# Kernel optimization log

Measured on AMD Instinct MI355X. Metric: run time of the kernel, lower is better.

The kernel has to match this reference:

```python
import jax, jax.numpy as jnp
import numpy as np

N_NODES = 50000
N_EDGES = 400000
F_IN = 128
HID = 64
HEADS = 8
N_CLASSES = 16
NEG_SLOPE = 0.2  # PyG GATConv default negative_slope


def _glorot(key, shape):
    fan_in, fan_out = shape[0], shape[-1]
    lim = jnp.sqrt(6.0 / (fan_in + fan_out))
    return jax.random.uniform(key, shape, jnp.float32, -lim, lim)


def setup_inputs() -> dict:
    key = jax.random.key(0)
    ks = jax.random.split(key, 16)
    x = jax.random.normal(ks[0], (N_NODES, F_IN), jnp.float32)
    edge_index = jax.random.randint(ks[1], (2, N_EDGES), 0, N_NODES, jnp.int64)
    # layer 0: F_IN -> HEADS*HID (concat)
    W0 = _glorot(ks[2], (F_IN, HEADS * HID))
    a_s0 = _glorot(ks[3], (HEADS, HID))
    a_d0 = _glorot(ks[4], (HEADS, HID))
    b0 = jnp.zeros((HEADS * HID,), jnp.float32)
    # layer 1: HEADS*HID -> HEADS*HID (concat)
    W1 = _glorot(ks[5], (HEADS * HID, HEADS * HID))
    a_s1 = _glorot(ks[6], (HEADS, HID))
    a_d1 = _glorot(ks[7], (HEADS, HID))
    b1 = jnp.zeros((HEADS * HID,), jnp.float32)
    # final layer: HEADS*HID -> N_CLASSES, heads=1, concat=False (mean over heads)
    W2 = _glorot(ks[8], (HEADS * HID, 1 * N_CLASSES))
    a_s2 = _glorot(ks[9], (1, N_CLASSES))
    a_d2 = _glorot(ks[10], (1, N_CLASSES))
    b2 = jnp.zeros((N_CLASSES,), jnp.float32)
    return {"x": x, "edge_index": edge_index,
            "W0": W0, "a_s0": a_s0, "a_d0": a_d0, "b0": b0,
            "W1": W1, "a_s1": a_s1, "a_d1": a_d1, "b1": b1,
            "W2": W2, "a_s2": a_s2, "a_d2": a_d2, "b2": b2}


def gat_conv(x, src, dst, W, a_src, a_dst, b, num_nodes, concat):
    """One PyG-style GATConv (self-loops already in src/dst).
    x: [N, F_in]; W: [F_in, H*C]; a_src/a_dst: [H, C]; b: [H*C] or [C]."""
    H, C = a_src.shape
    h = (x @ W).reshape(num_nodes, H, C)                    # [N,H,C]
    al_s = jnp.einsum('nhc,hc->nh', h, a_src)               # [N,H]
    al_d = jnp.einsum('nhc,hc->nh', h, a_dst)               # [N,H]
    e = jax.nn.leaky_relu(al_s[src] + al_d[dst], NEG_SLOPE) # [E,H]
    # scatter-softmax over incoming edges of each destination node
    m = jax.ops.segment_max(e, dst, num_segments=num_nodes)  # [N,H]
    ex = jnp.exp(e - m[dst])
    denom = jax.ops.segment_sum(ex, dst, num_segments=num_nodes)
    alpha = ex / denom[dst]                                  # [E,H]
    out = jax.ops.segment_sum(alpha[:, :, None] * h[src], dst,
                              num_segments=num_nodes)        # [N,H,C]
    if concat:
        return out.reshape(num_nodes, H * C) + b
    return out.mean(axis=1) + b


def reference(x, edge_index, W0, a_s0, a_d0, b0, W1, a_s1, a_d1, b1,
              W2, a_s2, a_d2, b2):
    N = x.shape[0]
    # PyG GATConv adds self-loops by default
    loops = jnp.arange(N, dtype=edge_index.dtype)
    src = jnp.concatenate([edge_index[0], loops])
    dst = jnp.concatenate([edge_index[1], loops])
    h = gat_conv(x, src, dst, W0, a_s0, a_d0, b0, N, concat=True)
    h = jax.nn.elu(h)  # dropout is identity in eval mode
    h = gat_conv(h, src, dst, W1, a_s1, a_d1, b1, N, concat=True)
    h = jax.nn.elu(h)
    return gat_conv(h, src, dst, W2, a_s2, a_d2, b2, N, concat=False)
```

## Files before the change

kernel.cpp:

```cpp
#include <hip/hip_runtime.h>

#define N_NODES 50000
#define N_EDGES 400000
#define E_TOT   450000
#define NEG 0.2f
#define NB_SCAN ((N_NODES + 255) / 256)
#define MAXD 64

typedef unsigned short ushort_t;
typedef __attribute__((ext_vector_type(8))) _Float16 half8;
typedef __attribute__((ext_vector_type(4))) float  f32x4;
typedef __attribute__((ext_vector_type(8))) unsigned short ushort8;

__device__ __forceinline__ ushort_t f2h(float f){
    _Float16 h = (_Float16)f;
    union { _Float16 h; ushort_t u; } v; v.h = h; return v.u;
}
__device__ __forceinline__ float h_lo(unsigned u){
    union { unsigned u; _Float16 h[2]; } v; v.u = u; return (float)v.h[0];
}
__device__ __forceinline__ float h_hi(unsigned u){
    union { unsigned u; _Float16 h[2]; } v; v.u = u; return (float)v.h[1];
}
__device__ __forceinline__ void gload_lds16(const void* g, void* l){
    __builtin_amdgcn_global_load_lds((const __attribute__((address_space(1))) void*)g,
                                     (__attribute__((address_space(3))) void*)l, 16, 0, 0);
}
__device__ __forceinline__ int wave_incl_scan(int v, int lane){
    #pragma unroll
    for(int off = 1; off < 64; off <<= 1){
        int t = __shfl_up(v, off, 64);
        if(lane >= off) v += t;
    }
    return v;
}


__global__ void cvt_all(const float* __restrict__ x, const float* __restrict__ W0,
                        const float* __restrict__ W1, const float* __restrict__ W2,
                        const int* __restrict__ ei,
                        ushort_t* __restrict__ xbf, ushort_t* __restrict__ W0t,
                        ushort_t* __restrict__ W1t, ushort_t* __restrict__ W2t,
                        int* __restrict__ deg){
    int i = blockIdx.x*256 + threadIdx.x;
    if(i < N_NODES*128) xbf[i] = f2h(x[i]);
    if(i < 512*128){ int n = i >> 7, k = i & 127; W0t[i] = f2h(W0[(size_t)k*512 + n]); }
    if(i < 512*512){ int n = i >> 9, k = i & 511; W1t[i] = f2h(W1[(size_t)k*512 + n]); }
    if(i < 16*512){ int n = i >> 9, k = i & 511; W2t[i] = f2h(W2[(size_t)k*16 + n]); }
    if(i < E_TOT){
        int dst = (i < N_EDGES) ? ei[N_EDGES + i] : (i - N_EDGES);
        atomicAdd(&deg[dst], 1);
    }
}


__global__ void alloc_rows(int* __restrict__ wofs, int* __restrict__ rs, int* __restrict__ re){
    int i = blockIdx.x*256 + threadIdx.x;
    int lane = threadIdx.x & 63;
    int d = (i < N_NODES) ? wofs[i] : 0;
    int incl = wave_incl_scan(d, lane);
    int tot = __shfl(incl, 63);
    int base;
    if(lane == 63) base = atomicAdd(&wofs[N_NODES], tot);
    base = __shfl(base, 63);
    int start = base + incl - d;
    if(i < N_NODES){ rs[i] = start; re[i] = start + d; wofs[i] = start; }
}

__global__ void scatter_edges(const int* __restrict__ ei, int* __restrict__ wofs,
                              int* __restrict__ csr){
    int e = blockIdx.x*256 + threadIdx.x;
    if(e >= E_TOT) return;
    int src, dst;
    if(e < N_EDGES){ src = ei[e]; dst = ei[N_EDGES + e]; }
    else { src = dst = e - N_EDGES; }
    int pos = atomicAdd(&wofs[dst], 1);
    csr[pos] = src;
}


template<int K>
__global__ __launch_bounds__(512, 2) void gemm_bt8(const ushort_t* __restrict__ A,
                                                   const ushort_t* __restrict__ Bt,
                                                   ushort_t* __restrict__ Cb,
                                                   const float* __restrict__ a_s,
                                                   const float* __restrict__ a_d,
                                                   float* __restrict__ als,
                                                   float* __restrict__ ald, int M){
    extern __shared__ ushort_t lds[];
    constexpr int NT = K / 64;
    int tid = threadIdx.x, wave = tid >> 6, lane = tid & 63;
    int wm = wave >> 2, wn = wave & 3;
    int row0 = blockIdx.y * 256;
    int col0 = blockIdx.x * 256;

    int lr = lane >> 3;
    int cs8 = ((lane & 7) ^ lr) << 3;
    int arows[4], brows[4];
    #pragma unroll
    for(int i = 0; i < 4; i++){
        int r = row0 + (wave << 5) + (i << 3) + lr;
        arows[i] = r < M ? r : M-1;
        brows[i] = col0 + (wave << 5) + (i << 3) + lr;
    }

    int l15 = lane & 15, fq = lane >> 4;
    int xr = (lane & 7) << 4;
    int xco0 = ((fq << 4)      ) ^ xr;
    int xco1 = (64 | (fq << 4)) ^ xr;

    f32x4 acc[8][4] = {};

    auto stage = [&](int nb, int kt, int i){
        ushort_t* la = lds + nb*16384 + (wave << 11) + (i << 9);
        ushort_t* lb = lds + 32768 + nb*16384 + (wave << 11) + (i << 9);
        gload_lds16(A  + (size_t)arows[i]*K + kt + cs8, la);
        gload_lds16(Bt + (size_t)brows[i]*K + kt + cs8, lb);
    };

    #pragma unroll
    for(int i = 0; i < 4; i++) stage(0, 0, i);

    for(int it = 0; it < NT; ++it){
        int b = it & 1;
        asm volatile("s_waitcnt vmcnt(0)" ::: "memory");
        __builtin_amdgcn_s_barrier();
        const char* Ac = (const char*)(lds + b*16384);
        const char* Bc = (const char*)(lds + 32768 + b*16384);
        #pragma unroll
        for(int p = 0; p < 4; ++p){
            if(it < NT-1 && p < 2){
                stage(b ^ 1, (it + 1) << 6, 2*p);
                stage(b ^ 1, (it + 1) << 6, 2*p + 1);
            }
            half8 aF[2][2], bF[4][2];
            #pragma unroll
            for(int m2 = 0; m2 < 2; m2++){
                int ro = (((wm << 7) + (((p << 1) | m2) << 4) + l15)) << 7;
                aF[m2][0] = *(const half8*)(Ac + ro + xco0);
                aF[m2][1] = *(const half8*)(Ac + ro + xco1);
            }
            #pragma unroll
            for(int nj = 0; nj < 4; nj++){
                int ro = (((wn << 6) + (nj << 4) + l15)) << 7;
                bF[nj][0] = *(const half8*)(Bc + ro + xco0);
                bF[nj][1] = *(const half8*)(Bc + ro + xco1);
            }
            __builtin_amdgcn_s_barrier();
            __builtin_amdgcn_s_setprio(1);
            #pragma unroll
            for(int m2 = 0; m2 < 2; m2++)
                #pragma unroll
                for(int nj = 0; nj < 4; nj++){
                    acc[(p<<1)|m2][nj] = __builtin_amdgcn_mfma_f32_16x16x32_f16(aF[m2][0], bF[nj][0], acc[(p<<1)|m2][nj], 0, 0, 0);
                    acc[(p<<1)|m2][nj] = __builtin_amdgcn_mfma_f32_16x16x32_f16(aF[m2][1], bF[nj][1], acc[(p<<1)|m2][nj], 0, 0, 0);
                }
            __builtin_amdgcn_s_setprio(0);
            __builtin_amdgcn_s_barrier();
        }
    }

    int head = (col0 >> 6) + wn;
    float asv[4], adv[4];
    #pragma unroll
    for(int nj = 0; nj < 4; nj++){
        int c = (head << 6) + (nj << 4) + l15;
        asv[nj] = a_s[c]; adv[nj] = a_d[c];
    }
    #pragma unroll
    for(int mi = 0; mi < 8; mi++){
        #pragma unroll
        for(int p2 = 0; p2 < 4; p2++){
            int r = row0 + (wm << 7) + (mi << 4) + (fq << 2) + p2;
            float ps = 0.f, pd = 0.f;
            if(r < M){
                ushort_t* cp = &Cb[(size_t)r*512 + (head << 6) + l15];
                #pragma unroll
                for(int nj = 0; nj < 4; nj++){
                    float v = acc[mi][nj][p2];
                    cp[nj << 4] = f2h(v);
                    ps += v*asv[nj]; pd += v*adv[nj];
                }
            }
            #pragma unroll
            for(int off = 1; off < 16; off <<= 1){
                ps += __shfl_xor(ps, off);
                pd += __shfl_xor(pd, off);
            }
            if(l15 == 0 && r < M){ als[r*8 + head] = ps; ald[r*8 + head] = pd; }
        }
    }
}


template<bool F2>
__global__ __launch_bounds__(256) void attn_agg(const ushort_t* __restrict__ h,
        const float* __restrict__ als, const float* __restrict__ ald,
        const int* __restrict__ rs, const int* __restrict__ re,
        const int* __restrict__ csr,
        const float* __restrict__ bias, ushort_t* __restrict__ out,
        const ushort_t* __restrict__ W2t, const float* __restrict__ a_s2,
        const float* __restrict__ a_d2, float* __restrict__ h2,
        float* __restrict__ als2, float* __restrict__ ald2){
    __shared__ float sm[4][8], sd[4][8];
    __shared__ float sex[4][MAXD][8];
    int wv = threadIdx.x >> 6, lane = threadIdx.x & 63;
    int n = blockIdx.x*4 + wv;
    int start = rs[n], end = re[n];

    int hd = lane & 7, e8 = lane >> 3;
    float aldv = ald[n*8 + hd];
    float lmax = -1e30f;
    for(int idx = start + e8; idx < end; idx += 8){
        int e = idx - start;
        int src = csr[idx];
        float v = als[src*8 + hd] + aldv;
        v = v > 0.f ? v : NEG*v;
        if(e < MAXD) sex[wv][e][hd] = v;
        lmax = fmaxf(lmax, v);
    }
    for(int off = 8; off < 64; off <<= 1) lmax = fmaxf(lmax, __shfl_xor(lmax, off));
    float lsum = 0.f;
    for(int idx = start + e8; idx < end; idx += 8){
        int e = idx - start;
        float v;
        if(e < MAXD) v = sex[wv][e][hd];
        else { int src = csr[idx]; v = als[src*8 + hd] + aldv; v = v > 0.f ? v : NEG*v; }
        float ex = __expf(v - lmax);
        if(e < MAXD) sex[wv][e][hd] = ex;
        lsum += ex;
    }
    for(int off = 8; off < 64; off <<= 1) lsum += __shfl_xor(lsum, off);
    if(lane < 8){ sm[wv][hd] = lmax; sd[wv][hd] = 1.f / lsum; }
    __syncthreads();

    int head = lane >> 3;
    float inv = sd[wv][head];
    float acc[8] = {};

    int cnt = end - start;
    int nmain = cnt < MAXD ? cnt : MAXD;
    int mend = start + nmain;
    int last = mend - 1;
    for(int idx = start; idx < mend; idx += 8){
        int ss[8]; uint4 pp[8]; float ee[8];
        #pragma unroll
        for(int k = 0; k < 8; k++){
            int j = idx + k;
            ss[k] = csr[j <= last ? j : last];
        }
        #pragma unroll
        for(int k = 0; k < 8; k++)
            pp[k] = *(const uint4*)&h[(size_t)ss[k]*512 + lane*8];
        #pragma unroll
        for(int k = 0; k < 8; k++){
            int j = idx + k;
            ee[k] = (j < mend) ? sex[wv][j-start][head] : 0.f;
        }
        #pragma unroll
        for(int k = 0; k < 8; k++){
            acc[0] += ee[k]*h_lo(pp[k].x); acc[1] += ee[k]*h_hi(pp[k].x);
            acc[2] += ee[k]*h_lo(pp[k].y); acc[3] += ee[k]*h_hi(pp[k].y);
            acc[4] += ee[k]*h_lo(pp[k].z); acc[5] += ee[k]*h_hi(pp[k].z);
            acc[6] += ee[k]*h_lo(pp[k].w); acc[7] += ee[k]*h_hi(pp[k].w);
        }
    }
    if(mend < end){
        float m = sm[wv][head];
        float aldn = ald[n*8 + head];
        for(int idx = mend; idx < end; idx++){
            int src = csr[idx];
            float v = als[src*8 + head] + aldn;
            v = v > 0.f ? v : NEG*v;
            float e0 = __expf(v - m);
            uint4 p = *(const uint4*)&h[(size_t)src*512 + lane*8];
            acc[0] += e0*h_lo(p.x); acc[1] += e0*h_hi(p.x);
            acc[2] += e0*h_lo(p.y); acc[3] += e0*h_hi(p.y);
            acc[4] += e0*h_lo(p.z); acc[5] += e0*h_hi(p.z);
            acc[6] += e0*h_lo(p.w); acc[7] += e0*h_hi(p.w);
        }
    }

    float vv[8];
    ushort8 o;
    #pragma unroll
    for(int j = 0; j < 8; j++){
        float v = acc[j]*inv + bias[lane*8 + j];
        v = v > 0.f ? v : (__expf(v) - 1.f);
        vv[j] = v;
        o[j] = f2h(v);
    }
    *(ushort8*)&out[(size_t)n*512 + lane*8] = o;

    if constexpr (F2){
        float ps = 0.f, pd = 0.f, yval = 0.f;
        #pragma unroll
        for(int c = 0; c < 16; c++){
            half8 wvv = *(const half8*)&W2t[c*512 + lane*8];
            float yc = vv[0]*(float)wvv[0] + vv[1]*(float)wvv[1]
                     + vv[2]*(float)wvv[2] + vv[3]*(float)wvv[3]
                     + vv[4]*(float)wvv[4] + vv[5]*(float)wvv[5]
                     + vv[6]*(float)wvv[6] + vv[7]*(float)wvv[7];
            #pragma unroll
            for(int off = 1; off < 64; off <<= 1) yc += __shfl_xor(yc, off);
            ps += yc * a_s2[c]; pd += yc * a_d2[c];
            if(lane == c) yval = yc;
        }
        if(lane < 16) h2[(size_t)n*16 + lane] = yval;
        if(lane == 0){ als2[n] = ps; ald2[n] = pd; }
    }
}

__global__ __launch_bounds__(256) void attn_agg2(const float* __restrict__ h2,
        const float* __restrict__ als, const float* __restrict__ ald,
        const int* __restrict__ rs, const int* __restrict__ re,
        const int* __restrict__ csr,
        const float* __restrict__ b2, float* __restrict__ out){
    __shared__ float sex2[16][MAXD+1];
    int wv = threadIdx.x >> 6, lane = threadIdx.x & 63;
    int q = lane >> 4, c = lane & 15;
    int slot = wv*4 + q;
    int n = blockIdx.x*16 + slot;
    int start = rs[n], end = re[n];
    float aldv = ald[n];
    int cnt = end - start;
    int nmain = cnt < MAXD ? cnt : MAXD;
    int mend = start + nmain;

    float lmax = -1e30f;
    for(int idx = start + c; idx < end; idx += 16){
        int e = idx - start;
        float v = als[csr[idx]] + aldv; v = v > 0.f ? v : NEG*v;
        if(e < MAXD) sex2[slot][e] = v;
        lmax = fmaxf(lmax, v);
    }
    #pragma unroll
    for(int off = 1; off < 16; off <<= 1) lmax = fmaxf(lmax, __shfl_xor(lmax, off));
    float lsum = 0.f;
    for(int idx = start + c; idx < end; idx += 16){
        int e = idx - start;
        float v;
        if(e < MAXD) v = sex2[slot][e];
        else { v = als[csr[idx]] + aldv; v = v > 0.f ? v : NEG*v; }
        float ex = __expf(v - lmax);
        if(e < MAXD) sex2[slot][e] = ex;
        lsum += ex;
    }
    #pragma unroll
    for(int off = 1; off < 16; off <<= 1) lsum += __shfl_xor(lsum, off);
    float inv = 1.f / lsum;

    float acc = 0.f;
    for(int idx = start; idx < mend; idx++){
        int src = csr[idx];
        float ex = sex2[slot][idx - start];
        acc += ex * h2[(size_t)src*16 + c];
    }
    for(int idx = mend; idx < end; idx++){
        int src = csr[idx];
        float v = als[src] + aldv; v = v > 0.f ? v : NEG*v;
        acc += __expf(v - lmax) * h2[(size_t)src*16 + c];
    }
    out[(size_t)n*16 + c] = acc*inv + b2[c];
}


extern "C" void kernel_launch(void* const* d_in, const int* in_sizes, int n_in,
                              void* d_out, int out_size, void* d_ws, size_t ws_size,
                              hipStream_t stream) {
    const float* x    = (const float*)d_in[0];
    const int*   ei   = (const int*)  d_in[1];
    const float* W0   = (const float*)d_in[2];
    const float* a_s0 = (const float*)d_in[3];
    const float* a_d0 = (const float*)d_in[4];
    const float* b0   = (const float*)d_in[5];
    const float* W1   = (const float*)d_in[6];
    const float* a_s1 = (const float*)d_in[7];
    const float* a_d1 = (const float*)d_in[8];
    const float* b1   = (const float*)d_in[9];
    const float* W2   = (const float*)d_in[10];
    const float* a_s2 = (const float*)d_in[11];
    const float* a_d2 = (const float*)d_in[12];
    const float* b2   = (const float*)d_in[13];
    float* out = (float*)d_out;

    char* w = (char*)d_ws;
    auto alloc = [&](size_t bytes){ void* p = (void*)w; w += (bytes + 255) & ~(size_t)255; return p; };
    int*      rs     = (int*)     alloc(N_NODES*sizeof(int));
    int*      re     = (int*)     alloc(N_NODES*sizeof(int));
    int*      wofs   = (int*)     alloc((N_NODES+1)*sizeof(int));
    int*      csr    = (int*)     alloc(E_TOT*sizeof(int));
    float*    als    = (float*)   alloc((size_t)N_NODES*8*sizeof(float));
    float*    ald    = (float*)   alloc((size_t)N_NODES*8*sizeof(float));
    float*    als2   = (float*)   alloc((size_t)N_NODES*sizeof(float));
    float*    ald2   = (float*)   alloc((size_t)N_NODES*sizeof(float));
    ushort_t* hb     = (ushort_t*)alloc((size_t)N_NODES*512*sizeof(ushort_t));
    ushort_t* hbf    = (ushort_t*)alloc((size_t)N_NODES*512*sizeof(ushort_t));
    ushort_t* xbf    = (ushort_t*)alloc((size_t)N_NODES*128*sizeof(ushort_t));
    ushort_t* W0t    = (ushort_t*)alloc((size_t)512*128*sizeof(ushort_t));
    ushort_t* W1t    = (ushort_t*)alloc((size_t)512*512*sizeof(ushort_t));
    ushort_t* W2t    = (ushort_t*)alloc((size_t)16*512*sizeof(ushort_t));
    float*    h2     = (float*)   alloc((size_t)N_NODES*16*sizeof(float));

    (void)hipFuncSetAttribute((const void*)gemm_bt8<128>,
                              hipFuncAttributeMaxDynamicSharedMemorySize, 131072);
    (void)hipFuncSetAttribute((const void*)gemm_bt8<512>,
                              hipFuncAttributeMaxDynamicSharedMemorySize, 131072);

    hipMemsetAsync(wofs, 0, (N_NODES+1)*sizeof(int), stream);
    cvt_all<<<(N_NODES*128+255)/256, 256, 0, stream>>>(x, W0, W1, W2, ei, xbf, W0t, W1t, W2t, wofs);

    alloc_rows<<<NB_SCAN, 256, 0, stream>>>(wofs, rs, re);
    scatter_edges<<<(E_TOT+255)/256, 256, 0, stream>>>(ei, wofs, csr);

    gemm_bt8<128><<<dim3(2, (N_NODES+255)/256), 512, 131072, stream>>>(xbf, W0t, hb, a_s0, a_d0, als, ald, N_NODES);
    attn_agg<false><<<N_NODES/4, 256, 0, stream>>>(hb, als, ald, rs, re, csr, b0, hbf,
                                                   nullptr, nullptr, nullptr, nullptr, nullptr, nullptr);

    gemm_bt8<512><<<dim3(2, (N_NODES+255)/256), 512, 131072, stream>>>(hbf, W1t, hb, a_s1, a_d1, als, ald, N_NODES);
    attn_agg<true><<<N_NODES/4, 256, 0, stream>>>(hb, als, ald, rs, re, csr, b1, hbf,
                                                  W2t, a_s2, a_d2, h2, als2, ald2);

    attn_agg2<<<N_NODES/16, 256, 0, stream>>>(h2, als2, ald2, rs, re, csr, b2, out);
}
```

Measured before the change: 442.9 us.

## Unfuse final projection into MFMA kernel and remap GEMM blocks for XCD locality

The 16-class projection of layer 2 used to run inside the aggregation epilogue as per-wave shuffle reductions. It now runs as a separate MFMA GEMM over the stored fp16 activations. The main GEMMs also move to a 1D grid whose block index is remapped so that consecutive tiles land on the same XCD, aiming for better L2 reuse of A rows. In exchange there is an extra kernel launch and an extra read of the 50000x512 activation buffer.

```diff
diff --git a/kernel.cpp b/kernel.cpp
--- a/kernel.cpp
+++ b/kernel.cpp
@@ -91,8 +91,13 @@
     constexpr int NT = K / 64;
     int tid = threadIdx.x, wave = tid >> 6, lane = tid & 63;
     int wm = wave >> 2, wn = wave & 3;
-    int row0 = blockIdx.y * 256;
-    int col0 = blockIdx.x * 256;
+
+    int s = blockIdx.x, nb = gridDim.x;
+    int cc = s & 7, kk = s >> 3;
+    int q = nb >> 3, rr = nb & 7;
+    int t = (cc < rr ? cc*(q+1) : rr*(q+1) + (cc-rr)*q) + kk;
+    int row0 = (t >> 1) * 256;
+    int col0 = (t & 1) * 256;
 
     int lr = lane >> 3;
     int cs8 = ((lane & 7) ^ lr) << 3;
@@ -111,9 +116,9 @@
 
     f32x4 acc[8][4] = {};
 
-    auto stage = [&](int nb, int kt, int i){
-        ushort_t* la = lds + nb*16384 + (wave << 11) + (i << 9);
-        ushort_t* lb = lds + 32768 + nb*16384 + (wave << 11) + (i << 9);
+    auto stage = [&](int nbuf, int kt, int i){
+        ushort_t* la = lds + nbuf*16384 + (wave << 11) + (i << 9);
+        ushort_t* lb = lds + 32768 + nbuf*16384 + (wave << 11) + (i << 9);
         gload_lds16(A  + (size_t)arows[i]*K + kt + cs8, la);
         gload_lds16(Bt + (size_t)brows[i]*K + kt + cs8, lb);
     };
@@ -193,15 +198,11 @@
 }
 
 
-template<bool F2>
 __global__ __launch_bounds__(256) void attn_agg(const ushort_t* __restrict__ h,
         const float* __restrict__ als, const float* __restrict__ ald,
         const int* __restrict__ rs, const int* __restrict__ re,
         const int* __restrict__ csr,
-        const float* __restrict__ bias, ushort_t* __restrict__ out,
-        const ushort_t* __restrict__ W2t, const float* __restrict__ a_s2,
-        const float* __restrict__ a_d2, float* __restrict__ h2,
-        float* __restrict__ als2, float* __restrict__ ald2){
+        const float* __restrict__ bias, ushort_t* __restrict__ out){
     __shared__ float sm[4][8], sd[4][8];
     __shared__ float sex[4][MAXD][8];
     int wv = threadIdx.x >> 6, lane = threadIdx.x & 63;
@@ -281,33 +282,53 @@
         }
     }
 
-    float vv[8];
     ushort8 o;
     #pragma unroll
     for(int j = 0; j < 8; j++){
         float v = acc[j]*inv + bias[lane*8 + j];
         v = v > 0.f ? v : (__expf(v) - 1.f);
-        vv[j] = v;
         o[j] = f2h(v);
     }
     *(ushort8*)&out[(size_t)n*512 + lane*8] = o;
-
-    if constexpr (F2){
-        float ps = 0.f, pd = 0.f, yval = 0.f;
-        #pragma unroll
-        for(int c = 0; c < 16; c++){
-            half8 wvv = *(const half8*)&W2t[c*512 + lane*8];
-            float yc = vv[0]*(float)wvv[0] + vv[1]*(float)wvv[1]
-                     + vv[2]*(float)wvv[2] + vv[3]*(float)wvv[3]
-                     + vv[4]*(float)wvv[4] + vv[5]*(float)wvv[5]
-                     + vv[6]*(float)wvv[6] + vv[7]*(float)wvv[7];
-            #pragma unroll
-            for(int off = 1; off < 64; off <<= 1) yc += __shfl_xor(yc, off);
-            ps += yc * a_s2[c]; pd += yc * a_d2[c];
-            if(lane == c) yval = yc;
-        }
-        if(lane < 16) h2[(size_t)n*16 + lane] = yval;
-        if(lane == 0){ als2[n] = ps; ald2[n] = pd; }
+}
+
+
+__global__ __launch_bounds__(256) void gemm2_mfma(const ushort_t* __restrict__ A,
+                                                  const ushort_t* __restrict__ W2t,
+                                                  const float* __restrict__ a_s2,
+                                                  const float* __restrict__ a_d2,
+                                                  float* __restrict__ C,
+                                                  float* __restrict__ als,
+                                                  float* __restrict__ ald){
+    int wave = threadIdx.x >> 6, lane = threadIdx.x & 63;
+    long row0 = (long)(blockIdx.x*4 + wave)*16;
+    int fr = lane & 15, fq = lane >> 4;
+    long ar = row0 + fr;
+    if(ar > N_NODES-1) ar = N_NODES-1;
+    const ushort_t* ap = A + ar*512 + fq*8;
+    const ushort_t* bp = W2t + (size_t)fr*512 + fq*8;
+    f32x4 acc = {};
+    #pragma unroll
+    for(int kt = 0; kt < 512; kt += 32){
+        half8 a = *(const half8*)(ap + kt);
+        half8 b = *(const half8*)(bp + kt);
+        acc = __builtin_amdgcn_mfma_f32_16x16x32_f16(a, b, acc, 0, 0, 0);
+    }
+    float as_ = a_s2[fr], ad_ = a_d2[fr];
+    #pragma unroll
+    for(int p = 0; p < 4; p++){
+        long r = row0 + fq*4 + p;
+        float v = acc[p];
+        float ps = v*as_, pd = v*ad_;
+        #pragma unroll
+        for(int off = 1; off < 16; off <<= 1){
+            ps += __shfl_xor(ps, off);
+            pd += __shfl_xor(pd, off);
+        }
+        if(r < N_NODES){
+            C[r*16 + fr] = v;
+            if(fr == 0){ als[r] = ps; ald[r] = pd; }
+        }
     }
 }
 
@@ -402,6 +423,8 @@
     ushort_t* W2t    = (ushort_t*)alloc((size_t)16*512*sizeof(ushort_t));
     float*    h2     = (float*)   alloc((size_t)N_NODES*16*sizeof(float));
 
+    const int NBLK = 2 * ((N_NODES + 255) / 256);
+
     (void)hipFuncSetAttribute((const void*)gemm_bt8<128>,
                               hipFuncAttributeMaxDynamicSharedMemorySize, 131072);
     (void)hipFuncSetAttribute((const void*)gemm_bt8<512>,
@@ -413,13 +436,12 @@
     alloc_rows<<<NB_SCAN, 256, 0, stream>>>(wofs, rs, re);
     scatter_edges<<<(E_TOT+255)/256, 256, 0, stream>>>(ei, wofs, csr);
 
-    gemm_bt8<128><<<dim3(2, (N_NODES+255)/256), 512, 131072, stream>>>(xbf, W0t, hb, a_s0, a_d0, als, ald, N_NODES);
-    attn_agg<false><<<N_NODES/4, 256, 0, stream>>>(hb, als, ald, rs, re, csr, b0, hbf,
-                                                   nullptr, nullptr, nullptr, nullptr, nullptr, nullptr);
-
-    gemm_bt8<512><<<dim3(2, (N_NODES+255)/256), 512, 131072, stream>>>(hbf, W1t, hb, a_s1, a_d1, als, ald, N_NODES);
-    attn_agg<true><<<N_NODES/4, 256, 0, stream>>>(hb, als, ald, rs, re, csr, b1, hbf,
-                                                  W2t, a_s2, a_d2, h2, als2, ald2);
-
+    gemm_bt8<128><<<NBLK, 512, 131072, stream>>>(xbf, W0t, hb, a_s0, a_d0, als, ald, N_NODES);
+    attn_agg<<<N_NODES/4, 256, 0, stream>>>(hb, als, ald, rs, re, csr, b0, hbf);
+
+    gemm_bt8<512><<<NBLK, 512, 131072, stream>>>(hbf, W1t, hb, a_s1, a_d1, als, ald, N_NODES);
+    attn_agg<<<N_NODES/4, 256, 0, stream>>>(hb, als, ald, rs, re, csr, b1, hbf);
+
+    gemm2_mfma<<<(N_NODES+63)/64, 256, 0, stream>>>(hbf, W2t, a_s2, a_d2, h2, als2, ald2);
     attn_agg2<<<N_NODES/16, 256, 0, stream>>>(h2, als2, ald2, rs, re, csr, b2, out);
 }
```

Measured after the change: 441.4 us. No clear change (-0.3%).
